# Performance work log

Measured on AMD Instinct MI355X. Metric: run time of the kernel, lower is better.

## Reference

```python
import jax, jax.numpy as jnp
import numpy as np

N_NODES = 50000
N_EDGES = 800000
N_PRED = 100000  # pos and neg each
D_IN = 256
D_HID = 128  # hard-coded hidden width of conv1
D_OUT = 128  # out_channels


def _lin_params(key, fan_in, fan_out, dtype=jnp.float32):
    kw, kb = jax.random.split(key)
    s = 1.0 / np.sqrt(fan_in)
    W = jax.random.uniform(kw, (fan_in, fan_out), dtype, -s, s)
    b = jax.random.uniform(kb, (fan_out,), dtype, -s, s)
    return W, b


def setup_inputs() -> dict:
    key = jax.random.key(0)
    ks = jax.random.split(key, 16)
    inp = {
        "x": jax.random.normal(ks[0], (N_NODES, D_IN), jnp.float32),
        "edge_index": jax.random.randint(ks[1], (2, N_EDGES), 0, N_NODES, jnp.int64),
        "pos_edge_index": jax.random.randint(ks[2], (2, N_PRED), 0, N_NODES, jnp.int64),
        "neg_edge_index": jax.random.randint(ks[3], (2, N_PRED), 0, N_NODES, jnp.int64),
    }
    # conv1: TransformerConv(D_IN -> D_HID), heads=1, root_weight=True
    inp["Wq1"], inp["bq1"] = _lin_params(ks[4], D_IN, D_HID)
    inp["Wk1"], inp["bk1"] = _lin_params(ks[5], D_IN, D_HID)
    inp["Wv1"], inp["bv1"] = _lin_params(ks[6], D_IN, D_HID)
    inp["Ws1"], inp["bs1"] = _lin_params(ks[7], D_IN, D_HID)
    # conv2: TransformerConv(D_HID -> D_OUT)
    inp["Wq2"], inp["bq2"] = _lin_params(ks[8], D_HID, D_OUT)
    inp["Wk2"], inp["bk2"] = _lin_params(ks[9], D_HID, D_OUT)
    inp["Wv2"], inp["bv2"] = _lin_params(ks[10], D_HID, D_OUT)
    inp["Ws2"], inp["bs2"] = _lin_params(ks[11], D_HID, D_OUT)
    # final edge scorer Linear(D_OUT, 1)
    inp["Wl"], inp["bl"] = _lin_params(ks[12], D_OUT, 1)
    return inp


def _transformer_conv(x, Wq, bq, Wk, bk, Wv, bv, Ws, bs, src, dst, n_nodes):
    # PyG TransformerConv, heads=1, concat=True, root_weight=True, no edge attrs.
    C = Wq.shape[1]
    q = x @ Wq + bq  # [N, C] queries (destination side)
    k = x @ Wk + bk  # [N, C] keys (source side)
    v = x @ Wv + bv  # [N, C] values (source side)
    # per-edge attention logits, softmax normalized over incoming edges of dst
    alpha = jnp.einsum("ec,ec->e", q[dst], k[src]) / jnp.sqrt(jnp.asarray(C, x.dtype))
    amax = jax.lax.stop_gradient(jax.ops.segment_max(alpha, dst, num_segments=n_nodes))
    ex = jnp.exp(alpha - amax[dst])
    den = jax.ops.segment_sum(ex, dst, num_segments=n_nodes)
    w = ex / den[dst]  # [E]
    agg = jax.ops.segment_sum(v[src] * w[:, None], dst, num_segments=n_nodes)  # [N, C]
    return agg + (x @ Ws + bs)  # skip connection (lin_skip)


def reference(x, edge_index, pos_edge_index, neg_edge_index,
              Wq1, bq1, Wk1, bk1, Wv1, bv1, Ws1, bs1,
              Wq2, bq2, Wk2, bk2, Wv2, bv2, Ws2, bs2,
              Wl, bl):
    src, dst = edge_index[0], edge_index[1]
    h = _transformer_conv(x, Wq1, bq1, Wk1, bk1, Wv1, bv1, Ws1, bs1, src, dst, N_NODES)
    h = jax.nn.relu(h)
    h = _transformer_conv(h, Wq2, bq2, Wk2, bk2, Wv2, bv2, Ws2, bs2, src, dst, N_NODES)
    ei = jnp.concatenate([pos_edge_index, neg_edge_index], axis=-1)  # [2, 2*N_PRED]
    prod = h[ei[0]] * h[ei[1]]  # [2*N_PRED, D_OUT]
    return (prod @ Wl + bl).squeeze(-1)  # [2*N_PRED]
```

## Files before the change

kernel.cpp:

```cpp
#include <hip/hip_runtime.h>
#include <cstdint>
#include <cstddef>

#define NN 50000
#define NE 800000
#define NP 100000

#define EPB    3125
#define NBUK   196

#define CVT_BLOCKS   12500
#define PACKW_BLOCKS 1024
#define RADIX1_BLOCKS 256

typedef _Float16 h8v __attribute__((ext_vector_type(8)));
typedef _Float16 h4v __attribute__((ext_vector_type(4)));
typedef _Float16 h2v __attribute__((ext_vector_type(2)));
typedef float    f4v __attribute__((ext_vector_type(4)));

#define ATTN_SCALE 0.088388347648318447f

__device__ inline void load_lds16(const void* gptr, void* ldsptr) {
  __builtin_amdgcn_global_load_lds(
      (const __attribute__((address_space(1))) void*)gptr,
      (__attribute__((address_space(3))) void*)ldsptr, 16, 0, 0);
}

__device__ inline float dot8(h8v a, h8v b, float c) {
  union U { h8v v; h2v p[4]; };
  U ua; ua.v = a;
  U ub; ub.v = b;
#if __has_builtin(__builtin_amdgcn_fdot2)
  c = __builtin_amdgcn_fdot2(ua.p[0], ub.p[0], c, false);
  c = __builtin_amdgcn_fdot2(ua.p[1], ub.p[1], c, false);
  c = __builtin_amdgcn_fdot2(ua.p[2], ub.p[2], c, false);
  c = __builtin_amdgcn_fdot2(ua.p[3], ub.p[3], c, false);
#else
#pragma unroll
  for (int j = 0; j < 8; ++j) c = fmaf((float)a[j], (float)b[j], c);
#endif
  return c;
}

__global__ __launch_bounds__(256) void prep_kernel(
    const float* __restrict__ x, _Float16* __restrict__ Xf,
    const float* __restrict__ Wq1, const float* __restrict__ Wk1,
    const float* __restrict__ Wv1, const float* __restrict__ Ws1,
    const float* __restrict__ Wq2, const float* __restrict__ Wk2,
    const float* __restrict__ Wv2, const float* __restrict__ Ws2,
    _Float16* __restrict__ WT1, _Float16* __restrict__ WT2,
    const int* __restrict__ dst, unsigned short* __restrict__ erank,
    int* __restrict__ blockcount) {
  __shared__ int cnt[256];
  int b = blockIdx.x;
  int tid = threadIdx.x;
  if (b < CVT_BLOCKS) {
    int i = b * 256 + tid;
    float4 xv = ((const float4*)x)[i];
    h4v o = {(_Float16)xv.x, (_Float16)xv.y, (_Float16)xv.z, (_Float16)xv.w};
    ((h4v*)Xf)[i] = o;
  } else if (b < CVT_BLOCKS + PACKW_BLOCKS) {
    int bb = b - CVT_BLOCKS;
    if (bb < 512) {
      int n = bb;
      const float* W;
      switch (n >> 7) {
        case 0:  W = Wq1; break;
        case 1:  W = Wk1; break;
        case 2:  W = Wv1; break;
        default: W = Ws1; break;
      }
      WT1[(size_t)n * 256 + tid] = (_Float16)W[(size_t)tid * 128 + (n & 127)];
    } else if (tid < 128) {
      int n = bb - 512;
      const float* W;
      switch (n >> 7) {
        case 0:  W = Wq2; break;
        case 1:  W = Wk2; break;
        case 2:  W = Wv2; break;
        default: W = Ws2; break;
      }
      WT2[(size_t)n * 128 + tid] = (_Float16)W[(size_t)tid * 128 + (n & 127)];
    }
  } else {
    int blk = b - CVT_BLOCKS - PACKW_BLOCKS;
    cnt[tid] = 0;
    __syncthreads();
    int base = blk * EPB;
    for (int i = tid; i < EPB; i += 256) {
      int e = base + i;
      erank[e] = (unsigned short)atomicAdd(&cnt[dst[e] >> 8], 1);
    }
    __syncthreads();
    blockcount[tid * 256 + blk] = cnt[tid];
  }
}

__global__ __launch_bounds__(256) void scan1_kernel(const int* __restrict__ deg,
                                                    int* __restrict__ loc,
                                                    int* __restrict__ bsum, int n) {
  __shared__ int sh[256];
  int tid = threadIdx.x;
  int i = blockIdx.x * 256 + tid;
  int val = (i < n) ? deg[i] : 0;
  sh[tid] = val;
  __syncthreads();
  for (int off = 1; off < 256; off <<= 1) {
    int add = (tid >= off) ? sh[tid - off] : 0;
    __syncthreads();
    sh[tid] += add;
    __syncthreads();
  }
  if (i < n) loc[i] = sh[tid] - val;
  if (tid == 255) bsum[blockIdx.x] = sh[255];
}

__global__ __launch_bounds__(256) void scan23_kernel(const int* __restrict__ loc,
                                                     const int* __restrict__ bsum,
                                                     int* __restrict__ outv,
                                                     int n, int E) {
  __shared__ int sh[256];
  int bid = blockIdx.x, tid = threadIdx.x;
  int pre = 0;
  for (int j = tid; j < bid; j += 256) pre += bsum[j];
  sh[tid] = pre;
  __syncthreads();
  for (int off = 128; off > 0; off >>= 1) {
    if (tid < off) sh[tid] += sh[tid + off];
    __syncthreads();
  }
  int base = sh[0];
  int i = bid * 256 + tid;
  if (i < n) outv[i] = loc[i] + base;
  if (bid == 0 && tid == 0) outv[n] = E;
}

__global__ __launch_bounds__(256) void radix2_kernel(
    const int* __restrict__ src, const int* __restrict__ dst,
    const int* __restrict__ bcscan, const unsigned short* __restrict__ erank,
    unsigned* __restrict__ tmp) {
  int blk = blockIdx.x, tid = threadIdx.x;
  int base = blk * EPB;
  for (int i = tid; i < EPB; i += 256) {
    int e = base + i;
    int d = dst[e];
    int pos = bcscan[(d >> 8) * 256 + blk] + (int)erank[e];
    tmp[pos] = (unsigned)src[e] | ((unsigned)(d & 255) << 16);
  }
}

__global__ __launch_bounds__(256) void radix3_kernel(
    const unsigned* __restrict__ tmp, const int* __restrict__ bcscan,
    unsigned short* __restrict__ rank2,
    int* __restrict__ offs, unsigned short* __restrict__ csr_src) {
  __shared__ int cnt[256];
  __shared__ int sh[256];
  int tid = threadIdx.x, bu = blockIdx.x;
  cnt[tid] = 0;
  __syncthreads();
  int bstart = bcscan[bu * 256];
  int bend   = bcscan[(bu + 1) * 256];
  for (int i = bstart + tid; i < bend; i += 256) {
    unsigned u = tmp[i];
    rank2[i] = (unsigned short)atomicAdd(&cnt[u >> 16], 1);
  }
  __syncthreads();
  int v = cnt[tid];
  sh[tid] = v;
  __syncthreads();
  for (int off = 1; off < 256; off <<= 1) {
    int add = (tid >= off) ? sh[tid - off] : 0;
    __syncthreads();
    sh[tid] += add;
    __syncthreads();
  }
  int excl = sh[tid] - v;
  int node = bu * 256 + tid;
  if (node < NN) offs[node] = bstart + excl;
  if (bu == 0 && tid == 0) offs[NN] = NE;
  __syncthreads();
  cnt[tid] = excl;
  __syncthreads();
  for (int i = bstart + tid; i < bend; i += 256) {
    unsigned u = tmp[i];
    csr_src[bstart + cnt[u >> 16] + (int)rank2[i]] = (unsigned short)(u & 0xffffu);
  }
}

__global__ __launch_bounds__(512) void gemm_all_kernel(
    const _Float16* __restrict__ A, int M, int K,
    const _Float16* __restrict__ BT,
    const float* __restrict__ bq, const float* __restrict__ bk,
    const float* __restrict__ bv, const float* __restrict__ bs,
    _Float16* __restrict__ Oq, _Float16* __restrict__ Okv,
    _Float16* __restrict__ Os) {
  __shared__ _Float16 As[128 * 64];
  __shared__ _Float16 Bs[512 * 64];

  const int tx = threadIdx.x;
  const int w = tx >> 6;
  const int lane = tx & 63;
  const int lr = lane & 15;
  const int q = lane >> 4;
  const int wm = w >> 2;
  const int wn = w & 3;
  const int row0 = blockIdx.x * 128;

  f4v acc[4][8];
#pragma unroll
  for (int i = 0; i < 4; ++i)
#pragma unroll
    for (int j = 0; j < 8; ++j) acc[i][j] = (f4v){0.f, 0.f, 0.f, 0.f};

  for (int k0 = 0; k0 < K; k0 += 64) {
    __syncthreads();
#pragma unroll
    for (int o = 0; o < 2; ++o) {
      int i = o * 8 + w;
      int r = i * 8 + (lane >> 3);
      int cl = (lane & 7) ^ (r & 7);
      int gr = row0 + r;
      if (gr > M - 1) gr = M - 1;
      load_lds16(A + (size_t)gr * K + k0 + cl * 8, &As[i * 8 * 64]);
    }
#pragma unroll
    for (int o = 0; o < 8; ++o) {
      int i = o * 8 + w;
      int r = i * 8 + (lane >> 3);
      int cl = (lane & 7) ^ (r & 7);
      load_lds16(BT + (size_t)r * K + k0 + cl * 8, &Bs[i * 8 * 64]);
    }
    __syncthreads();

#pragma unroll
    for (int kk = 0; kk < 2; ++kk) {
      h8v af[4], bf[8];
#pragma unroll
      for (int t = 0; t < 4; ++t) {
        int row = wm * 64 + t * 16 + lr;
        af[t] = *(const h8v*)&As[row * 64 + (((kk * 4 + q) ^ (row & 7)) * 8)];
      }
#pragma unroll
      for (int u = 0; u < 8; ++u) {
        int col = wn * 128 + u * 16 + lr;
        bf[u] = *(const h8v*)&Bs[col * 64 + (((kk * 4 + q) ^ (col & 7)) * 8)];
      }
#pragma unroll
      for (int mt = 0; mt < 4; ++mt)
#pragma unroll
        for (int nt = 0; nt < 8; ++nt)
          acc[mt][nt] = __builtin_amdgcn_mfma_f32_16x16x32_f16(af[mt], bf[nt],
                                                               acc[mt][nt], 0, 0, 0);
    }
  }

  const float* bp = (wn == 0) ? bq : (wn == 1) ? bk : (wn == 2) ? bv : bs;
#pragma unroll
  for (int half = 0; half < 2; ++half) {
    __syncthreads();
    if (wm == half) {
#pragma unroll
      for (int nt = 0; nt < 8; ++nt) {
        int col = wn * 128 + nt * 16 + lr;
        float bval = bp[nt * 16 + lr];
#pragma unroll
        for (int mt = 0; mt < 4; ++mt)
#pragma unroll
          for (int reg = 0; reg < 4; ++reg) {
            int r = mt * 16 + q * 4 + reg;
            Bs[r * 512 + col] = (_Float16)(acc[mt][nt][reg] + bval);
          }
      }
    }
    __syncthreads();
#pragma unroll
    for (int i = 0; i < 8; ++i) {
      int sl = i * 512 + tx;
      int rr = sl >> 6;
      int c8 = sl & 63;
      int col = c8 * 8;
      int grow = row0 + half * 64 + rr;
      if (grow < M) {
        int p = c8 >> 4;
        int cp = col & 127;
        _Float16* dstp;
        switch (p) {
          case 0:  dstp = Oq  + (size_t)grow * 128 + cp;       break;
          case 1:  dstp = Okv + (size_t)grow * 256 + cp;       break;
          case 2:  dstp = Okv + (size_t)grow * 256 + 128 + cp; break;
          default: dstp = Os  + (size_t)grow * 128 + cp;       break;
        }
        *(h8v*)dstp = *(const h8v*)&Bs[rr * 512 + col];
      }
    }
  }
}

__global__ __launch_bounds__(256) void attn_fused_kernel(
    const _Float16* __restrict__ qf, const _Float16* __restrict__ kvf,
    const _Float16* __restrict__ sf,
    const int* __restrict__ offs, const unsigned short* __restrict__ csr_src,
    _Float16* __restrict__ hf, int n_nodes, int do_relu) {
  int node = (int)((blockIdx.x * 256u + threadIdx.x) >> 6);
  if (node >= n_nodes) return;
  int lane = threadIdx.x & 63;
  int g = lane >> 4;
  int t = lane & 15;

  h8v qv = *(const h8v*)(qf + (size_t)node * 128 + t * 8);
  int beg = offs[node], end = offs[node + 1];

  float den = 0.f;
  float acc[8];
#pragma unroll
  for (int j = 0; j < 8; ++j) acc[j] = 0.f;

  int e = beg + g;
  for (; e + 4 < end; e += 8) {
    int sn0 = csr_src[e];
    int sn1 = csr_src[e + 4];
    const _Float16* r0 = kvf + (size_t)sn0 * 256 + t * 8;
    const _Float16* r1 = kvf + (size_t)sn1 * 256 + t * 8;
    h8v k0 = *(const h8v*)r0, v0 = *(const h8v*)(r0 + 128);
    h8v k1 = *(const h8v*)r1, v1 = *(const h8v*)(r1 + 128);
    float p0 = dot8(qv, k0, 0.f);
    float p1 = dot8(qv, k1, 0.f);
    p0 += __shfl_xor(p0, 1); p1 += __shfl_xor(p1, 1);
    p0 += __shfl_xor(p0, 2); p1 += __shfl_xor(p1, 2);
    p0 += __shfl_xor(p0, 4); p1 += __shfl_xor(p1, 4);
    p0 += __shfl_xor(p0, 8); p1 += __shfl_xor(p1, 8);
    float w0 = __expf(p0 * ATTN_SCALE);
    float w1 = __expf(p1 * ATTN_SCALE);
    den += w0 + w1;
#pragma unroll
    for (int j = 0; j < 8; ++j) {
      acc[j] = fmaf(w0, (float)v0[j], acc[j]);
      acc[j] = fmaf(w1, (float)v1[j], acc[j]);
    }
  }
  if (e < end) {
    int sn0 = csr_src[e];
    const _Float16* r0 = kvf + (size_t)sn0 * 256 + t * 8;
    h8v k0 = *(const h8v*)r0, v0 = *(const h8v*)(r0 + 128);
    float p0 = dot8(qv, k0, 0.f);
    p0 += __shfl_xor(p0, 1);
    p0 += __shfl_xor(p0, 2);
    p0 += __shfl_xor(p0, 4);
    p0 += __shfl_xor(p0, 8);
    float w0 = __expf(p0 * ATTN_SCALE);
    den += w0;
#pragma unroll
    for (int j = 0; j < 8; ++j) acc[j] = fmaf(w0, (float)v0[j], acc[j]);
  }

#pragma unroll
  for (int j = 0; j < 8; ++j) {
    acc[j] += __shfl_xor(acc[j], 16);
    acc[j] += __shfl_xor(acc[j], 32);
  }
  den += __shfl_xor(den, 16);
  den += __shfl_xor(den, 32);

  if (g == 0) {
    float inv = (end > beg) ? 1.f / den : 0.f;
    h8v sk = *(const h8v*)(sf + (size_t)node * 128 + t * 8);
    h8v of;
#pragma unroll
    for (int j = 0; j < 8; ++j) {
      float o = fmaf(acc[j], inv, (float)sk[j]);
      if (do_relu) o = fmaxf(o, 0.f);
      of[j] = (_Float16)o;
    }
    *(h8v*)(hf + (size_t)node * 128 + t * 8) = of;
  }
}

__global__ __launch_bounds__(256) void scorer_kernel(
    const _Float16* __restrict__ hf,
    const int* __restrict__ pos0, const int* __restrict__ pos1,
    const int* __restrict__ neg0, const int* __restrict__ neg1,
    const float* __restrict__ Wl, const float* __restrict__ bl,
    float* __restrict__ out, int npred) {
  int eid = (int)((blockIdx.x * 256u + threadIdx.x) >> 4);
  if (eid >= 2 * npred) return;
  int t = threadIdx.x & 15;

  int a, b;
  if (eid < npred) { a = pos0[eid]; b = pos1[eid]; }
  else             { a = neg0[eid - npred]; b = neg1[eid - npred]; }

  h8v ha = *(const h8v*)(hf + (size_t)a * 128 + t * 8);
  h8v hb = *(const h8v*)(hf + (size_t)b * 128 + t * 8);
  const float4* wp = (const float4*)(Wl + t * 8);
  float4 w0 = wp[0], w1 = wp[1];
  float wl[8] = {w0.x, w0.y, w0.z, w0.w, w1.x, w1.y, w1.z, w1.w};
  float p = 0.f;
#pragma unroll
  for (int j = 0; j < 8; ++j)
    p = fmaf((float)ha[j] * (float)hb[j], wl[j], p);
  p += __shfl_xor(p, 1);
  p += __shfl_xor(p, 2);
  p += __shfl_xor(p, 4);
  p += __shfl_xor(p, 8);
  if (t == 0) out[eid] = p + bl[0];
}

extern "C" void kernel_launch(void* const* d_in, const int* in_sizes, int n_in,
                              void* d_out, int out_size, void* d_ws, size_t ws_size,
                              hipStream_t stream) {
  const float* x   = (const float*)d_in[0];
  const int*   ei  = (const int*)d_in[1];
  const int*   pos = (const int*)d_in[2];
  const int*   neg = (const int*)d_in[3];
  const float* Wq1 = (const float*)d_in[4];  const float* bq1 = (const float*)d_in[5];
  const float* Wk1 = (const float*)d_in[6];  const float* bk1 = (const float*)d_in[7];
  const float* Wv1 = (const float*)d_in[8];  const float* bv1 = (const float*)d_in[9];
  const float* Ws1 = (const float*)d_in[10]; const float* bs1 = (const float*)d_in[11];
  const float* Wq2 = (const float*)d_in[12]; const float* bq2 = (const float*)d_in[13];
  const float* Wk2 = (const float*)d_in[14]; const float* bk2 = (const float*)d_in[15];
  const float* Wv2 = (const float*)d_in[16]; const float* bv2 = (const float*)d_in[17];
  const float* Ws2 = (const float*)d_in[18]; const float* bs2 = (const float*)d_in[19];
  const float* Wl  = (const float*)d_in[20]; const float* bl  = (const float*)d_in[21];
  float* out = (float*)d_out;

  const size_t NODE_C = (size_t)NN * 128;
  char* p = (char*)d_ws;
  _Float16* qf  = (_Float16*)p; p += NODE_C * 2;
  _Float16* kvf = (_Float16*)p; p += NODE_C * 4;
  _Float16* sf  = (_Float16*)p; p += NODE_C * 2;
  _Float16* h1  = (_Float16*)p; p += NODE_C * 2;
  _Float16* h2  = (_Float16*)p; p += NODE_C * 2;
  _Float16* Xf  = (_Float16*)p; p += (size_t)NN * 256 * 2;
  _Float16* WT1 = (_Float16*)p; p += 512 * 256 * 2;
  _Float16* WT2 = (_Float16*)p; p += 512 * 128 * 2;
  unsigned short* erank = (unsigned short*)p; p += (size_t)NE * 2;
  unsigned short* rank2 = (unsigned short*)p; p += (size_t)NE * 2;
  unsigned* tmp = (unsigned*)p;  p += (size_t)NE * 4;
  int* bc     = (int*)p;         p += 65536 * 4;
  int* bcloc  = (int*)p;         p += 65536 * 4;
  int* bcbs   = (int*)p;         p += 256 * 4;
  int* bcscan = (int*)p;         p += 65544 * 4;
  int* offs   = (int*)p;         p += (size_t)(NN + 8) * 4;
  unsigned short* csr_src = (unsigned short*)p; p += (size_t)NE * 2;

  const int* e_src = ei;
  const int* e_dst = ei + NE;

  prep_kernel<<<CVT_BLOCKS + PACKW_BLOCKS + RADIX1_BLOCKS, 256, 0, stream>>>(
      x, Xf, Wq1, Wk1, Wv1, Ws1, Wq2, Wk2, Wv2, Ws2, WT1, WT2,
      e_dst, erank, bc);

  scan1_kernel<<<256, 256, 0, stream>>>(bc, bcloc, bcbs, 65536);
  scan23_kernel<<<256, 256, 0, stream>>>(bcloc, bcbs, bcscan, 65536, NE);

  radix2_kernel<<<256, 256, 0, stream>>>(e_src, e_dst, bcscan, erank, tmp);
  radix3_kernel<<<NBUK, 256, 0, stream>>>(tmp, bcscan, rank2, offs, csr_src);

  int ggrid = (NN + 127) / 128;
  int attn_blocks = (NN * 64 + 255) / 256;

  gemm_all_kernel<<<ggrid, 512, 0, stream>>>(Xf, NN, 256, WT1,
                                             bq1, bk1, bv1, bs1, qf, kvf, sf);
  attn_fused_kernel<<<attn_blocks, 256, 0, stream>>>(
      qf, kvf, sf, offs, csr_src, h1, NN, 1);

  gemm_all_kernel<<<ggrid, 512, 0, stream>>>(h1, NN, 128, WT2,
                                             bq2, bk2, bv2, bs2, qf, kvf, sf);
  attn_fused_kernel<<<attn_blocks, 256, 0, stream>>>(
      qf, kvf, sf, offs, csr_src, h2, NN, 0);

  scorer_kernel<<<(2 * NP * 16 + 255) / 256, 256, 0, stream>>>(
      h2, pos, pos + NP, neg, neg + NP, Wl, bl, out, NP);
}
```

Measured before the change: 350.8 us.

## Make GEMM persistent per projection with resident weight slice, prefetch CSR indices

```diff
diff --git a/kernel.cpp b/kernel.cpp
--- a/kernel.cpp
+++ b/kernel.cpp
@@ -187,110 +187,120 @@
   }
 }
 
-__global__ __launch_bounds__(512) void gemm_all_kernel(
+__global__ __launch_bounds__(256) void gemm_pb_kernel(
     const _Float16* __restrict__ A, int M, int K,
     const _Float16* __restrict__ BT,
     const float* __restrict__ bq, const float* __restrict__ bk,
     const float* __restrict__ bv, const float* __restrict__ bs,
     _Float16* __restrict__ Oq, _Float16* __restrict__ Okv,
     _Float16* __restrict__ Os) {
-  __shared__ _Float16 As[128 * 64];
-  __shared__ _Float16 Bs[512 * 64];
+  extern __shared__ _Float16 smem[];
+  _Float16* Bs = smem;
+  _Float16* As = smem + 128 * K;
 
   const int tx = threadIdx.x;
   const int w = tx >> 6;
   const int lane = tx & 63;
   const int lr = lane & 15;
   const int q = lane >> 4;
-  const int wm = w >> 2;
-  const int wn = w & 3;
-  const int row0 = blockIdx.x * 128;
-
-  f4v acc[4][8];
-#pragma unroll
-  for (int i = 0; i < 4; ++i)
-#pragma unroll
-    for (int j = 0; j < 8; ++j) acc[i][j] = (f4v){0.f, 0.f, 0.f, 0.f};
-
-  for (int k0 = 0; k0 < K; k0 += 64) {
-    __syncthreads();
-#pragma unroll
-    for (int o = 0; o < 2; ++o) {
-      int i = o * 8 + w;
-      int r = i * 8 + (lane >> 3);
-      int cl = (lane & 7) ^ (r & 7);
-      int gr = row0 + r;
-      if (gr > M - 1) gr = M - 1;
-      load_lds16(A + (size_t)gr * K + k0 + cl * 8, &As[i * 8 * 64]);
-    }
-#pragma unroll
-    for (int o = 0; o < 8; ++o) {
-      int i = o * 8 + w;
-      int r = i * 8 + (lane >> 3);
-      int cl = (lane & 7) ^ (r & 7);
-      load_lds16(BT + (size_t)r * K + k0 + cl * 8, &Bs[i * 8 * 64]);
-    }
-    __syncthreads();
-
-#pragma unroll
-    for (int kk = 0; kk < 2; ++kk) {
-      h8v af[4], bf[8];
-#pragma unroll
-      for (int t = 0; t < 4; ++t) {
-        int row = wm * 64 + t * 16 + lr;
-        af[t] = *(const h8v*)&As[row * 64 + (((kk * 4 + q) ^ (row & 7)) * 8)];
-      }
-#pragma unroll
-      for (int u = 0; u < 8; ++u) {
-        int col = wn * 128 + u * 16 + lr;
-        bf[u] = *(const h8v*)&Bs[col * 64 + (((kk * 4 + q) ^ (col & 7)) * 8)];
-      }
-#pragma unroll
-      for (int mt = 0; mt < 4; ++mt)
-#pragma unroll
-        for (int nt = 0; nt < 8; ++nt)
-          acc[mt][nt] = __builtin_amdgcn_mfma_f32_16x16x32_f16(af[mt], bf[nt],
-                                                               acc[mt][nt], 0, 0, 0);
-    }
-  }
-
-  const float* bp = (wn == 0) ? bq : (wn == 1) ? bk : (wn == 2) ? bv : bs;
-#pragma unroll
-  for (int half = 0; half < 2; ++half) {
-    __syncthreads();
-    if (wm == half) {
-#pragma unroll
-      for (int nt = 0; nt < 8; ++nt) {
-        int col = wn * 128 + nt * 16 + lr;
-        float bval = bp[nt * 16 + lr];
+  const int wm = w >> 1, wn = w & 1;
+  const int p = blockIdx.y;
+  const int rowshift = (K == 256) ? 5 : 4;
+  const int rowchunks = K >> 3;
+
+  {
+    const _Float16* Bp = BT + (size_t)p * 128 * K;
+    int total = 128 * rowchunks;
+    for (int s0 = w * 64; s0 < total; s0 += 256) {
+      int s = s0 + lane;
+      int r = s >> rowshift;
+      int sc = s & (rowchunks - 1);
+      int g = (sc & ~7) | ((sc & 7) ^ (r & 7));
+      load_lds16(Bp + (size_t)r * K + g * 8, &Bs[(size_t)s0 * 8]);
+    }
+  }
+
+  const float* bp = (p == 0) ? bq : (p == 1) ? bk : (p == 2) ? bv : bs;
+
+  for (int t = 0; t < 4; ++t) {
+    int tile = t * 98 + blockIdx.x;
+    int row0 = tile * 128;
+    if (row0 >= M) break;
+
+    f4v acc[4][4];
+#pragma unroll
+    for (int i = 0; i < 4; ++i)
+#pragma unroll
+      for (int j = 0; j < 4; ++j) acc[i][j] = (f4v){0.f, 0.f, 0.f, 0.f};
+
+    for (int k0 = 0; k0 < K; k0 += 64) {
+      __syncthreads();
+#pragma unroll
+      for (int o = 0; o < 4; ++o) {
+        int i = o * 4 + w;
+        int r = i * 8 + (lane >> 3);
+        int cl = (lane & 7) ^ (r & 7);
+        int gr = row0 + r;
+        if (gr > M - 1) gr = M - 1;
+        load_lds16(A + (size_t)gr * K + k0 + cl * 8, &As[i * 8 * 64]);
+      }
+      __syncthreads();
+
+#pragma unroll
+      for (int kk = 0; kk < 2; ++kk) {
+        h8v af[4], bf[4];
+#pragma unroll
+        for (int tt = 0; tt < 4; ++tt) {
+          int row = wm * 64 + tt * 16 + lr;
+          af[tt] = *(const h8v*)&As[row * 64 + (((kk * 4 + q) ^ (row & 7)) * 8)];
+          int col = wn * 64 + tt * 16 + lr;
+          int ck = (k0 >> 3) + kk * 4 + q;
+          int swz = (ck & ~7) | ((ck & 7) ^ (col & 7));
+          bf[tt] = *(const h8v*)&Bs[(size_t)col * K + swz * 8];
+        }
 #pragma unroll
         for (int mt = 0; mt < 4; ++mt)
 #pragma unroll
-          for (int reg = 0; reg < 4; ++reg) {
-            int r = mt * 16 + q * 4 + reg;
-            Bs[r * 512 + col] = (_Float16)(acc[mt][nt][reg] + bval);
+          for (int nt = 0; nt < 4; ++nt)
+            acc[mt][nt] = __builtin_amdgcn_mfma_f32_16x16x32_f16(af[mt], bf[nt],
+                                                                 acc[mt][nt], 0, 0, 0);
+      }
+    }
+
+#pragma unroll
+    for (int half = 0; half < 2; ++half) {
+      __syncthreads();
+      if (wm == half) {
+#pragma unroll
+        for (int nt = 0; nt < 4; ++nt) {
+          int col = wn * 64 + nt * 16 + lr;
+          float bval = bp[col];
+#pragma unroll
+          for (int mt = 0; mt < 4; ++mt)
+#pragma unroll
+            for (int reg = 0; reg < 4; ++reg) {
+              int r = mt * 16 + q * 4 + reg;
+              As[r * 128 + col] = (_Float16)(acc[mt][nt][reg] + bval);
+            }
+        }
+      }
+      __syncthreads();
+#pragma unroll
+      for (int i = 0; i < 4; ++i) {
+        int sl = i * 256 + tx;
+        int rr = sl >> 4;
+        int col = (sl & 15) * 8;
+        int grow = row0 + half * 64 + rr;
+        if (grow < M) {
+          _Float16* dstp;
+          switch (p) {
+            case 0:  dstp = Oq  + (size_t)grow * 128 + col;       break;
+            case 1:  dstp = Okv + (size_t)grow * 256 + col;       break;
+            case 2:  dstp = Okv + (size_t)grow * 256 + 128 + col; break;
+            default: dstp = Os  + (size_t)grow * 128 + col;       break;
           }
-      }
-    }
-    __syncthreads();
-#pragma unroll
-    for (int i = 0; i < 8; ++i) {
-      int sl = i * 512 + tx;
-      int rr = sl >> 6;
-      int c8 = sl & 63;
-      int col = c8 * 8;
-      int grow = row0 + half * 64 + rr;
-      if (grow < M) {
-        int p = c8 >> 4;
-        int cp = col & 127;
-        _Float16* dstp;
-        switch (p) {
-          case 0:  dstp = Oq  + (size_t)grow * 128 + cp;       break;
-          case 1:  dstp = Okv + (size_t)grow * 256 + cp;       break;
-          case 2:  dstp = Okv + (size_t)grow * 256 + 128 + cp; break;
-          default: dstp = Os  + (size_t)grow * 128 + cp;       break;
+          *(h8v*)dstp = *(const h8v*)&As[rr * 128 + col];
         }
-        *(h8v*)dstp = *(const h8v*)&Bs[rr * 512 + col];
       }
     }
   }
@@ -316,13 +326,17 @@
   for (int j = 0; j < 8; ++j) acc[j] = 0.f;
 
   int e = beg + g;
+  int sn0 = 0, sn1 = 0;
+  if (e < end) sn0 = csr_src[e];
+  if (e + 4 < end) sn1 = csr_src[e + 4];
+
   for (; e + 4 < end; e += 8) {
-    int sn0 = csr_src[e];
-    int sn1 = csr_src[e + 4];
     const _Float16* r0 = kvf + (size_t)sn0 * 256 + t * 8;
     const _Float16* r1 = kvf + (size_t)sn1 * 256 + t * 8;
     h8v k0 = *(const h8v*)r0, v0 = *(const h8v*)(r0 + 128);
     h8v k1 = *(const h8v*)r1, v1 = *(const h8v*)(r1 + 128);
+    int nn0 = (e + 8  < end) ? (int)csr_src[e + 8]  : 0;
+    int nn1 = (e + 12 < end) ? (int)csr_src[e + 12] : 0;
     float p0 = dot8(qv, k0, 0.f);
     float p1 = dot8(qv, k1, 0.f);
     p0 += __shfl_xor(p0, 1); p1 += __shfl_xor(p1, 1);
@@ -337,9 +351,9 @@
       acc[j] = fmaf(w0, (float)v0[j], acc[j]);
       acc[j] = fmaf(w1, (float)v1[j], acc[j]);
     }
+    sn0 = nn0; sn1 = nn1;
   }
   if (e < end) {
-    int sn0 = csr_src[e];
     const _Float16* r0 = kvf + (size_t)sn0 * 256 + t * 8;
     h8v k0 = *(const h8v*)r0, v0 = *(const h8v*)(r0 + 128);
     float p0 = dot8(qv, k0, 0.f);
@@ -456,16 +470,18 @@
   radix2_kernel<<<256, 256, 0, stream>>>(e_src, e_dst, bcscan, erank, tmp);
   radix3_kernel<<<NBUK, 256, 0, stream>>>(tmp, bcscan, rank2, offs, csr_src);
 
-  int ggrid = (NN + 127) / 128;
+  dim3 ggrid(98, 4);
   int attn_blocks = (NN * 64 + 255) / 256;
-
-  gemm_all_kernel<<<ggrid, 512, 0, stream>>>(Xf, NN, 256, WT1,
-                                             bq1, bk1, bv1, bs1, qf, kvf, sf);
+  size_t lds1 = (size_t)128 * (256 + 64) * 2;
+  size_t lds2 = (size_t)128 * (128 + 64) * 2;
+
+  gemm_pb_kernel<<<ggrid, 256, lds1, stream>>>(Xf, NN, 256, WT1,
+                                               bq1, bk1, bv1, bs1, qf, kvf, sf);
   attn_fused_kernel<<<attn_blocks, 256, 0, stream>>>(
       qf, kvf, sf, offs, csr_src, h1, NN, 1);
 
-  gemm_all_kernel<<<ggrid, 512, 0, stream>>>(h1, NN, 128, WT2,
-                                             bq2, bk2, bv2, bs2, qf, kvf, sf);
+  gemm_pb_kernel<<<ggrid, 256, lds2, stream>>>(h1, NN, 128, WT2,
+                                               bq2, bk2, bv2, bs2, qf, kvf, sf);
   attn_fused_kernel<<<attn_blocks, 256, 0, stream>>>(
       qf, kvf, sf, offs, csr_src, h2, NN, 0);
 
```

New measurement: 350.7 us. About the same (-0.0%).
